# Kernel optimization log

Hardware: AMD Instinct MI355X
Metric: run time of the kernel (lower is better)

Reference implementation:

```python
import jax, jax.numpy as jnp
import numpy as np

N_NODES = 50000
N_EDGES = 800000
IN_CH = 128
HID = 128
NUM_GRAPHS = 512
BN_EPS = 1e-5


def setup_inputs() -> dict:
    key = jax.random.key(0)
    ks = jax.random.split(key, 16)
    x = jax.random.normal(ks[0], (N_NODES, IN_CH), dtype=jnp.float32)
    edge_index = jax.random.randint(ks[1], (2, N_EDGES), 0, N_NODES, dtype=jnp.int64)
    batch = jnp.sort(jax.random.randint(ks[2], (N_NODES,), 0, NUM_GRAPHS, dtype=jnp.int64))

    def glorot(k, shape):
        fan_in = shape[1]
        return jax.random.normal(k, shape, dtype=jnp.float32) / jnp.sqrt(jnp.float32(fan_in))

    # SAGEConv1: lin_l (aggr path, with bias), lin_r (root path, no bias)
    W1l = glorot(ks[3], (HID, IN_CH)); b1 = jnp.zeros((HID,), jnp.float32)
    W1r = glorot(ks[4], (HID, IN_CH))
    # SAGEConv2
    W2l = glorot(ks[5], (HID, HID)); b2 = jnp.zeros((HID,), jnp.float32)
    W2r = glorot(ks[6], (HID, HID))
    # MLP tail
    lin1_w = glorot(ks[7], (HID, HID)); lin1_b = jnp.zeros((HID,), jnp.float32)
    lin2_w = glorot(ks[8], (2, HID)); lin2_b = jnp.zeros((2,), jnp.float32)
    # BatchNorm1d (eval mode, running stats)
    gamma = jnp.ones((HID,), jnp.float32)
    beta = jnp.zeros((HID,), jnp.float32)
    running_mean = jax.random.normal(ks[9], (HID,), dtype=jnp.float32) * 0.1
    running_var = jax.random.uniform(ks[10], (HID,), dtype=jnp.float32, minval=0.5, maxval=1.5)
    return {
        "x": x, "edge_index": edge_index, "batch": batch,
        "W1l": W1l, "b1": b1, "W1r": W1r,
        "W2l": W2l, "b2": b2, "W2r": W2r,
        "lin1_w": lin1_w, "lin1_b": lin1_b,
        "lin2_w": lin2_w, "lin2_b": lin2_b,
        "gamma": gamma, "beta": beta,
        "running_mean": running_mean, "running_var": running_var,
    }


def _sage_conv(x, src, dst, Wl, bl, Wr):
    # mean-aggregate neighbor features (message flows src -> dst)
    n = x.shape[0]
    agg = jax.ops.segment_sum(x[src], dst, num_segments=n)  # [N, d]
    cnt = jax.ops.segment_sum(jnp.ones((src.shape[0], 1), x.dtype), dst, num_segments=n)
    mean = agg / jnp.maximum(cnt, 1.0)
    return mean @ Wl.T + bl + x @ Wr.T


def reference(x, edge_index, batch, W1l, b1, W1r, W2l, b2, W2r,
              lin1_w, lin1_b, lin2_w, lin2_b, gamma, beta,
              running_mean, running_var):
    src, dst = edge_index[0], edge_index[1]
    h = _sage_conv(x, src, dst, W1l, b1, W1r)      # [N, HID]
    h = _sage_conv(h, src, dst, W2l, b2, W2r)      # [N, HID]
    h = jax.ops.segment_sum(h, batch, num_segments=NUM_GRAPHS)  # global_add_pool -> [G, HID]
    h = h @ lin1_w.T + lin1_b
    # BatchNorm1d in eval mode (running stats)
    h = (h - running_mean) * jax.lax.rsqrt(running_var + BN_EPS) * gamma + beta
    h = jax.nn.relu(h)
    h = h @ lin2_w.T + lin2_b                      # [G, 2]
    # Dropout is identity in eval mode
    return h
```

## Files before the change

### kernel.cpp

```cpp
#include <hip/hip_runtime.h>
#include <hip/hip_bf16.h>

#define NN 50000
#define NE 800000
#define HID 128
#define NG 512
#define BN_EPS 1e-5f

typedef __attribute__((ext_vector_type(8))) short bf16x8;
typedef __attribute__((ext_vector_type(4))) float f32x4;

__device__ __forceinline__ ushort f2bf(float f) {
    uint u = __float_as_uint(f);
    uint r = (u + 0x7fffu + ((u >> 16) & 1u)) >> 16;
    return (ushort)r;
}
__device__ __forceinline__ float bf_lo(uint v) { return __uint_as_float(v << 16); }
__device__ __forceinline__ float bf_hi(uint v) { return __uint_as_float(v & 0xffff0000u); }

#define HIST_BLOCKS 782
#define CONV_BLOCKS 6250
#define WPREP_BLOCKS 32
#define POOLZ_BLOCKS 64
#define PH_GRID (HIST_BLOCKS + CONV_BLOCKS + WPREP_BLOCKS + POOLZ_BLOCKS)

__global__ __launch_bounds__(256) void prep_hist_kernel(const int* __restrict__ ei,
                                                        int* __restrict__ deg,
                                                        int* __restrict__ rank,
                                                        const float* __restrict__ x,
                                                        ushort* __restrict__ xb,
                                                        const float* __restrict__ W0,
                                                        const float* __restrict__ W1,
                                                        const float* __restrict__ W2,
                                                        const float* __restrict__ W3,
                                                        ushort* __restrict__ Wp,
                                                        float* __restrict__ pooled) {
    uint b = blockIdx.x;
    if (b < HIST_BLOCKS) {
        int e4 = b * 256 + threadIdx.x;
        if (e4 < NE / 4) {
            int4 dst = ((const int4*)(ei + NE))[e4];
            int4 rk;
            rk.x = atomicAdd(&deg[dst.x], 1);
            rk.y = atomicAdd(&deg[dst.y], 1);
            rk.z = atomicAdd(&deg[dst.z], 1);
            rk.w = atomicAdd(&deg[dst.w], 1);
            ((int4*)rank)[e4] = rk;
        }
    } else if (b < HIST_BLOCKS + CONV_BLOCKS) {
        int i = (b - HIST_BLOCKS) * 256 + threadIdx.x;
        float4 v = ((const float4*)x)[i];
        ushort4 o;
        o.x = f2bf(v.x);
        o.y = f2bf(v.y);
        o.z = f2bf(v.z);
        o.w = f2bf(v.w);
        ((ushort4*)xb)[i] = o;
    } else if (b < HIST_BLOCKS + CONV_BLOCKS + WPREP_BLOCKS) {
        int wu = (b - HIST_BLOCKS - CONV_BLOCKS) * 4 + (threadIdx.x >> 6);
        if (wu >= 128) return;
        int lane = threadIdx.x & 63;
        int m = wu >> 5;
        int g = wu & 31;
        int tile = g >> 2;
        int chunk = g & 3;
        const float* W = (m == 0) ? W0 : (m == 1) ? W1 : (m == 2) ? W2 : W3;
        int col = tile * 16 + (lane & 15);
        int k0 = chunk * 32 + (lane >> 4) * 8;
        ushort* dst = Wp + ((size_t)wu * 64 + lane) * 8;
#pragma unroll
        for (int j = 0; j < 8; ++j) dst[j] = f2bf(W[col * HID + k0 + j]);
    } else {
        int i = (b - HIST_BLOCKS - CONV_BLOCKS - WPREP_BLOCKS) * 256 + threadIdx.x;
        ((float4*)pooled)[i] = make_float4(0.f, 0.f, 0.f, 0.f);
    }
}

__global__ __launch_bounds__(256) void scan1_kernel(const int* __restrict__ deg,
                                                    int* __restrict__ row_start,
                                                    int* __restrict__ bsums, int n) {
    __shared__ int wsum[4];
    int i = blockIdx.x * 256 + threadIdx.x;
    int lane = threadIdx.x & 63;
    int wid = threadIdx.x >> 6;
    int v = (i < n) ? deg[i] : 0;
    int sc = v;
#pragma unroll
    for (int off = 1; off < 64; off <<= 1) {
        int t = __shfl_up(sc, off);
        if (lane >= off) sc += t;
    }
    if (lane == 63) wsum[wid] = sc;
    __syncthreads();
    int wpre = 0;
#pragma unroll
    for (int k = 0; k < 4; ++k) wpre += (k < wid) ? wsum[k] : 0;
    if (i < n) row_start[i] = wpre + sc - v;
    if (threadIdx.x == 255) bsums[blockIdx.x] = wpre + sc;
}

__global__ __launch_bounds__(256) void scan23_kernel(int* __restrict__ row_start,
                                                     const int* __restrict__ bsums, int n) {
    __shared__ int sred[4];
    int v = (threadIdx.x < blockIdx.x) ? bsums[threadIdx.x] : 0;
#pragma unroll
    for (int off = 32; off > 0; off >>= 1) v += __shfl_xor(v, off);
    if ((threadIdx.x & 63) == 0) sred[threadIdx.x >> 6] = v;
    __syncthreads();
    int total = sred[0] + sred[1] + sred[2] + sred[3];
    int i = blockIdx.x * 256 + threadIdx.x;
    if (i < n) row_start[i] += total;
}

__global__ __launch_bounds__(256) void fill_kernel(const int* __restrict__ ei,
                                                   const int* __restrict__ row_start,
                                                   const int* __restrict__ rank,
                                                   ushort* __restrict__ srclist) {
    int e4 = blockIdx.x * 256 + threadIdx.x;
    if (e4 >= NE / 4) return;
    int4 src = ((const int4*)ei)[e4];
    int4 dst = ((const int4*)(ei + NE))[e4];
    int4 rk = ((const int4*)rank)[e4];
    int p0 = row_start[dst.x] + rk.x;
    int p1 = row_start[dst.y] + rk.y;
    int p2 = row_start[dst.z] + rk.z;
    int p3 = row_start[dst.w] + rk.w;
    srclist[p0] = (ushort)src.x;
    srclist[p1] = (ushort)src.y;
    srclist[p2] = (ushort)src.z;
    srclist[p3] = (ushort)src.w;
}

__global__ __launch_bounds__(256) void aggregate_kernel(const ushort* __restrict__ feat,
                                                        const int* __restrict__ row_start,
                                                        const int* __restrict__ deg,
                                                        const ushort* __restrict__ srclist,
                                                        ushort* __restrict__ mean, int n) {
    int node = blockIdx.x * 4 + (threadIdx.x >> 6);
    if (node >= n) return;
    int lane = threadIdx.x & 63;
    int cl = lane & 15;
    int sub = lane >> 4;
    const uint4* fb = (const uint4*)feat;
    int s0 = row_start[node];
    int d = deg[node];

    float a[8];
#pragma unroll
    for (int i = 0; i < 8; ++i) a[i] = 0.f;

    int j = 0;
    for (; j + 16 <= d; j += 16) {
        int i0 = srclist[s0 + j + sub];
        int i1 = srclist[s0 + j + 4 + sub];
        int i2 = srclist[s0 + j + 8 + sub];
        int i3 = srclist[s0 + j + 12 + sub];
        uint4 v0 = fb[(size_t)i0 * 16 + cl];
        uint4 v1 = fb[(size_t)i1 * 16 + cl];
        uint4 v2 = fb[(size_t)i2 * 16 + cl];
        uint4 v3 = fb[(size_t)i3 * 16 + cl];
        a[0] += (bf_lo(v0.x) + bf_lo(v1.x)) + (bf_lo(v2.x) + bf_lo(v3.x));
        a[1] += (bf_hi(v0.x) + bf_hi(v1.x)) + (bf_hi(v2.x) + bf_hi(v3.x));
        a[2] += (bf_lo(v0.y) + bf_lo(v1.y)) + (bf_lo(v2.y) + bf_lo(v3.y));
        a[3] += (bf_hi(v0.y) + bf_hi(v1.y)) + (bf_hi(v2.y) + bf_hi(v3.y));
        a[4] += (bf_lo(v0.z) + bf_lo(v1.z)) + (bf_lo(v2.z) + bf_lo(v3.z));
        a[5] += (bf_hi(v0.z) + bf_hi(v1.z)) + (bf_hi(v2.z) + bf_hi(v3.z));
        a[6] += (bf_lo(v0.w) + bf_lo(v1.w)) + (bf_lo(v2.w) + bf_lo(v3.w));
        a[7] += (bf_hi(v0.w) + bf_hi(v1.w)) + (bf_hi(v2.w) + bf_hi(v3.w));
    }
    if (j < d) {
        int dm1 = d - 1;
        int k0 = j + sub;
        int k1 = j + 4 + sub;
        int k2 = j + 8 + sub;
        int k3 = j + 12 + sub;
        int i0 = srclist[s0 + min(k0, dm1)];
        int i1 = srclist[s0 + min(k1, dm1)];
        int i2 = srclist[s0 + min(k2, dm1)];
        int i3 = srclist[s0 + min(k3, dm1)];
        uint4 v0 = fb[(size_t)i0 * 16 + cl];
        uint4 v1 = fb[(size_t)i1 * 16 + cl];
        uint4 v2 = fb[(size_t)i2 * 16 + cl];
        uint4 v3 = fb[(size_t)i3 * 16 + cl];
        float m0 = (k0 < d) ? 1.f : 0.f;
        float m1 = (k1 < d) ? 1.f : 0.f;
        float m2 = (k2 < d) ? 1.f : 0.f;
        float m3 = (k3 < d) ? 1.f : 0.f;
        a[0] += m0 * bf_lo(v0.x) + m1 * bf_lo(v1.x) + m2 * bf_lo(v2.x) + m3 * bf_lo(v3.x);
        a[1] += m0 * bf_hi(v0.x) + m1 * bf_hi(v1.x) + m2 * bf_hi(v2.x) + m3 * bf_hi(v3.x);
        a[2] += m0 * bf_lo(v0.y) + m1 * bf_lo(v1.y) + m2 * bf_lo(v2.y) + m3 * bf_lo(v3.y);
        a[3] += m0 * bf_hi(v0.y) + m1 * bf_hi(v1.y) + m2 * bf_hi(v2.y) + m3 * bf_hi(v3.y);
        a[4] += m0 * bf_lo(v0.z) + m1 * bf_lo(v1.z) + m2 * bf_lo(v2.z) + m3 * bf_lo(v3.z);
        a[5] += m0 * bf_hi(v0.z) + m1 * bf_hi(v1.z) + m2 * bf_hi(v2.z) + m3 * bf_hi(v3.z);
        a[6] += m0 * bf_lo(v0.w) + m1 * bf_lo(v1.w) + m2 * bf_lo(v2.w) + m3 * bf_lo(v3.w);
        a[7] += m0 * bf_hi(v0.w) + m1 * bf_hi(v1.w) + m2 * bf_hi(v2.w) + m3 * bf_hi(v3.w);
    }

#pragma unroll
    for (int i = 0; i < 8; ++i) {
        float v = a[i];
        v += __shfl_xor(v, 16);
        v += __shfl_xor(v, 32);
        a[i] = v;
    }

    if (sub == 0) {
        float inv = 1.0f / fmaxf((float)d, 1.0f);
        uint4 o;
        o.x = (uint)f2bf(a[0] * inv) | ((uint)f2bf(a[1] * inv) << 16);
        o.y = (uint)f2bf(a[2] * inv) | ((uint)f2bf(a[3] * inv) << 16);
        o.z = (uint)f2bf(a[4] * inv) | ((uint)f2bf(a[5] * inv) << 16);
        o.w = (uint)f2bf(a[6] * inv) | ((uint)f2bf(a[7] * inv) << 16);
        ((uint4*)mean)[(size_t)node * 16 + cl] = o;
    }
}

template <bool POOL>
__global__ __launch_bounds__(256) void sage_gemm_mfma(const ushort* __restrict__ Amean,
                                                      const ushort* __restrict__ Aroot,
                                                      const ushort* __restrict__ WpL,
                                                      const float* __restrict__ bias,
                                                      const int* __restrict__ batch,
                                                      void* __restrict__ outv, int nwaves) {
    int w = blockIdx.x * 4 + (threadIdx.x >> 6);
    if (w >= nwaves) return;
    int lane = threadIdx.x & 63;
    int mrow = lane & 15;
    int quad = lane >> 4;
    int r0 = w * 16;

    f32x4 acc[8];
#pragma unroll
    for (int t = 0; t < 8; ++t) acc[t] = (f32x4){0.f, 0.f, 0.f, 0.f};

    const ushort* arow_m = Amean + ((size_t)(r0 + mrow)) * HID + quad * 8;
    const ushort* arow_r = Aroot + ((size_t)(r0 + mrow)) * HID + quad * 8;

#pragma unroll
    for (int half = 0; half < 2; ++half) {
        const ushort* arow = half ? arow_r : arow_m;
        const ushort* wb = WpL + (size_t)half * 16384 + (size_t)lane * 8;
#pragma unroll
        for (int c = 0; c < 4; ++c) {
            bf16x8 a = *(const bf16x8*)(arow + c * 32);
#pragma unroll
            for (int t = 0; t < 8; ++t) {
                bf16x8 b = *(const bf16x8*)(wb + (size_t)(t * 4 + c) * 512);
                acc[t] = __builtin_amdgcn_mfma_f32_16x16x32_bf16(a, b, acc[t], 0, 0, 0);
            }
        }
    }

    if (POOL) {
        float* pooled = (float*)outv;
        int rbase = r0 + quad * 4;
        int g0 = batch[rbase + 0];
        int g1 = batch[rbase + 1];
        int g2 = batch[rbase + 2];
        int g3 = batch[rbase + 3];
#pragma unroll
        for (int t = 0; t < 8; ++t) {
            int col = t * 16 + mrow;
            float bv = bias[col];
            float v0 = acc[t][0] + bv;
            float v1 = acc[t][1] + bv;
            float v2 = acc[t][2] + bv;
            float v3 = acc[t][3] + bv;
            int cg = g0;
            float s = v0;
            if (g1 == cg) s += v1; else { atomicAdd(&pooled[(size_t)cg * HID + col], s); cg = g1; s = v1; }
            if (g2 == cg) s += v2; else { atomicAdd(&pooled[(size_t)cg * HID + col], s); cg = g2; s = v2; }
            if (g3 == cg) s += v3; else { atomicAdd(&pooled[(size_t)cg * HID + col], s); cg = g3; s = v3; }
            atomicAdd(&pooled[(size_t)cg * HID + col], s);
        }
    } else {
        ushort* out = (ushort*)outv;
#pragma unroll
        for (int t = 0; t < 8; ++t) {
            int col = t * 16 + mrow;
            float bv = bias[col];
#pragma unroll
            for (int r = 0; r < 4; ++r) {
                int row = r0 + quad * 4 + r;
                out[(size_t)row * HID + col] = f2bf(acc[t][r] + bv);
            }
        }
    }
}

__global__ __launch_bounds__(128) void tail_kernel(const float* __restrict__ pooled,
                                                   const float* __restrict__ lin1_w,
                                                   const float* __restrict__ lin1_b,
                                                   const float* __restrict__ lin2_w,
                                                   const float* __restrict__ lin2_b,
                                                   const float* __restrict__ gamma,
                                                   const float* __restrict__ beta,
                                                   const float* __restrict__ rmean,
                                                   const float* __restrict__ rvar,
                                                   float* __restrict__ out) {
    __shared__ float Wt[64 * 128];
    __shared__ float p[128];
    __shared__ float tbuf[128];
    int g = blockIdx.x;
    int c = threadIdx.x;
    p[c] = pooled[g * HID + c];
    float acc = lin1_b[c];
    int kk = c & 63;
    int chalf = c >> 6;
    for (int k0 = 0; k0 < 128; k0 += 64) {
        __syncthreads();
        for (int i = 0; i < 64; ++i) {
            int crow = i * 2 + chalf;
            float v = lin1_w[crow * HID + k0 + kk];
            Wt[kk * 128 + (crow ^ (kk & 31))] = v;
        }
        __syncthreads();
#pragma unroll
        for (int k = 0; k < 64; ++k) {
            acc += p[k0 + k] * Wt[k * 128 + (c ^ (k & 31))];
        }
    }
    float v = (acc - rmean[c]) * rsqrtf(rvar[c] + BN_EPS) * gamma[c] + beta[c];
    v = fmaxf(v, 0.f);
    tbuf[c] = v;
    __syncthreads();
    int j = c >> 6;
    int lane = c & 63;
    float partial = tbuf[lane] * lin2_w[j * HID + lane] +
                    tbuf[lane + 64] * lin2_w[j * HID + lane + 64];
    for (int off = 32; off > 0; off >>= 1) partial += __shfl_down(partial, off);
    if (lane == 0) out[g * 2 + j] = partial + lin2_b[j];
}

extern "C" void kernel_launch(void* const* d_in, const int* in_sizes, int n_in,
                              void* d_out, int out_size, void* d_ws, size_t ws_size,
                              hipStream_t stream) {
    const float* x = (const float*)d_in[0];
    const int* ei = (const int*)d_in[1];
    const int* batch = (const int*)d_in[2];
    const float* W1l = (const float*)d_in[3];
    const float* b1 = (const float*)d_in[4];
    const float* W1r = (const float*)d_in[5];
    const float* W2l = (const float*)d_in[6];
    const float* b2 = (const float*)d_in[7];
    const float* W2r = (const float*)d_in[8];
    const float* lin1_w = (const float*)d_in[9];
    const float* lin1_b = (const float*)d_in[10];
    const float* lin2_w = (const float*)d_in[11];
    const float* lin2_b = (const float*)d_in[12];
    const float* gamma = (const float*)d_in[13];
    const float* beta = (const float*)d_in[14];
    const float* rmean = (const float*)d_in[15];
    const float* rvar = (const float*)d_in[16];
    float* out = (float*)d_out;

    const int N = NN, E = NE;
    const int NWAVES = N / 16;

    char* p = (char*)d_ws;
    auto carve = [&](size_t bytes) {
        void* r = (void*)p;
        p += (bytes + 255) & ~(size_t)255;
        return r;
    };
    int* deg = (int*)carve((size_t)N * 4);
    int* row_start = (int*)carve((size_t)N * 4);
    int* bsums = (int*)carve(1024 * 4);
    int* rank = (int*)carve((size_t)E * 4);
    ushort* srclist = (ushort*)carve((size_t)E * 2 + 64);
    ushort* xb = (ushort*)carve((size_t)N * HID * 2);
    ushort* meanb = (ushort*)carve((size_t)N * HID * 2);
    ushort* h1 = (ushort*)carve((size_t)N * HID * 2);
    float* pooled = (float*)carve((size_t)NG * HID * 4);
    ushort* Wp = (ushort*)carve(4 * 32 * 64 * 8 * 2);

    hipMemsetAsync(deg, 0, (size_t)N * 4, stream);

    prep_hist_kernel<<<PH_GRID, 256, 0, stream>>>(ei, deg, rank, x, xb,
                                                  W1l, W1r, W2l, W2r, Wp, pooled);

    const int scanBlocks = (N + 255) / 256;
    scan1_kernel<<<scanBlocks, 256, 0, stream>>>(deg, row_start, bsums, N);
    scan23_kernel<<<scanBlocks, 256, 0, stream>>>(row_start, bsums, N);
    fill_kernel<<<(E / 4 + 255) / 256, 256, 0, stream>>>(ei, row_start, rank, srclist);

    aggregate_kernel<<<(N + 3) / 4, 256, 0, stream>>>(xb, row_start, deg, srclist, meanb, N);
    sage_gemm_mfma<false><<<(NWAVES + 3) / 4, 256, 0, stream>>>(meanb, xb, Wp, b1, nullptr, h1,
                                                                NWAVES);
    aggregate_kernel<<<(N + 3) / 4, 256, 0, stream>>>(h1, row_start, deg, srclist, meanb, N);
    sage_gemm_mfma<true><<<(NWAVES + 3) / 4, 256, 0, stream>>>(meanb, h1, Wp + 32768, b2, batch,
                                                               pooled, NWAVES);
    tail_kernel<<<NG, 128, 0, stream>>>(pooled, lin1_w, lin1_b, lin2_w, lin2_b,
                                        gamma, beta, rmean, rvar, out);
}
```

Baseline: 259.2 us.

## Replace global atomic degree histogram with per-chunk shared-memory histograms

The edge-degree histogram now runs as 128 blocks, each counting a 12500-edge chunk over half the node range. Counts are packed as 16-bit pairs in LDS (50KB per block), so the global atomics and the memset of deg go away. A new chunkscan kernel does a column-wise prefix over the 64 chunks to produce per-chunk offsets and total degrees, and fill adds the chunk offset to the rank. This trades contended global atomics for an extra kernel and a 6.4MB offset table. The large static LDS array is also allocated by the conversion and weight-prep blocks, which may reduce their occupancy.

```diff
diff --git a/kernel.cpp b/kernel.cpp
--- a/kernel.cpp
+++ b/kernel.cpp
@@ -18,15 +18,19 @@
 __device__ __forceinline__ float bf_lo(uint v) { return __uint_as_float(v << 16); }
 __device__ __forceinline__ float bf_hi(uint v) { return __uint_as_float(v & 0xffff0000u); }
 
-#define HIST_BLOCKS 782
+#define NCH 64
+#define CHE 12500
+#define HRNG 25000
+#define HWORDS 12500
+#define HIST_BLOCKS 128
 #define CONV_BLOCKS 6250
 #define WPREP_BLOCKS 32
 #define POOLZ_BLOCKS 64
 #define PH_GRID (HIST_BLOCKS + CONV_BLOCKS + WPREP_BLOCKS + POOLZ_BLOCKS)
 
 __global__ __launch_bounds__(256) void prep_hist_kernel(const int* __restrict__ ei,
-                                                        int* __restrict__ deg,
-                                                        int* __restrict__ rank,
+                                                        ushort* __restrict__ rank,
+                                                        ushort* __restrict__ blockcnt,
                                                         const float* __restrict__ x,
                                                         ushort* __restrict__ xb,
                                                         const float* __restrict__ W0,
@@ -35,18 +39,27 @@
                                                         const float* __restrict__ W3,
                                                         ushort* __restrict__ Wp,
                                                         float* __restrict__ pooled) {
+    __shared__ uint hh[HWORDS];
     uint b = blockIdx.x;
     if (b < HIST_BLOCKS) {
-        int e4 = b * 256 + threadIdx.x;
-        if (e4 < NE / 4) {
-            int4 dst = ((const int4*)(ei + NE))[e4];
-            int4 rk;
-            rk.x = atomicAdd(&deg[dst.x], 1);
-            rk.y = atomicAdd(&deg[dst.y], 1);
-            rk.z = atomicAdd(&deg[dst.z], 1);
-            rk.w = atomicAdd(&deg[dst.w], 1);
-            ((int4*)rank)[e4] = rk;
-        }
+        int c = b >> 1;
+        int r = b & 1;
+        for (int i = threadIdx.x; i < HWORDS; i += 256) hh[i] = 0;
+        __syncthreads();
+        int base = c * CHE;
+        int lo = r * HRNG;
+        for (int k = threadIdx.x; k < CHE; k += 256) {
+            int d = ei[NE + base + k];
+            int local = d - lo;
+            if ((unsigned)local < (unsigned)HRNG) {
+                uint sh = (local & 1) << 4;
+                uint old = atomicAdd(&hh[local >> 1], 1u << sh);
+                rank[base + k] = (ushort)((old >> sh) & 0xffffu);
+            }
+        }
+        __syncthreads();
+        uint* dstw = (uint*)(blockcnt + (size_t)c * NN) + r * HWORDS;
+        for (int i = threadIdx.x; i < HWORDS; i += 256) dstw[i] = hh[i];
     } else if (b < HIST_BLOCKS + CONV_BLOCKS) {
         int i = (b - HIST_BLOCKS) * 256 + threadIdx.x;
         float4 v = ((const float4*)x)[i];
@@ -76,6 +89,22 @@
     }
 }
 
+__global__ __launch_bounds__(256) void chunkscan_kernel(ushort* __restrict__ blockcnt,
+                                                        int* __restrict__ deg) {
+    int t = blockIdx.x * 256 + threadIdx.x;
+    if (t >= NN / 2) return;
+    uint run_lo = 0, run_hi = 0;
+    uint* col = (uint*)blockcnt + t;
+#pragma unroll 4
+    for (int c = 0; c < NCH; ++c) {
+        uint w = col[(size_t)c * (NN / 2)];
+        col[(size_t)c * (NN / 2)] = run_lo | (run_hi << 16);
+        run_lo += w & 0xffffu;
+        run_hi += w >> 16;
+    }
+    ((int2*)deg)[t] = make_int2((int)run_lo, (int)run_hi);
+}
+
 __global__ __launch_bounds__(256) void scan1_kernel(const int* __restrict__ deg,
                                                     int* __restrict__ row_start,
                                                     int* __restrict__ bsums, int n) {
@@ -114,17 +143,20 @@
 
 __global__ __launch_bounds__(256) void fill_kernel(const int* __restrict__ ei,
                                                    const int* __restrict__ row_start,
-                                                   const int* __restrict__ rank,
+                                                   const ushort* __restrict__ rank,
+                                                   const ushort* __restrict__ blockcnt,
                                                    ushort* __restrict__ srclist) {
     int e4 = blockIdx.x * 256 + threadIdx.x;
     if (e4 >= NE / 4) return;
     int4 src = ((const int4*)ei)[e4];
     int4 dst = ((const int4*)(ei + NE))[e4];
-    int4 rk = ((const int4*)rank)[e4];
-    int p0 = row_start[dst.x] + rk.x;
-    int p1 = row_start[dst.y] + rk.y;
-    int p2 = row_start[dst.z] + rk.z;
-    int p3 = row_start[dst.w] + rk.w;
+    ushort4 rk = ((const ushort4*)rank)[e4];
+    int c = e4 / (CHE / 4);
+    const ushort* off = blockcnt + (size_t)c * NN;
+    int p0 = row_start[dst.x] + off[dst.x] + rk.x;
+    int p1 = row_start[dst.y] + off[dst.y] + rk.y;
+    int p2 = row_start[dst.z] + off[dst.z] + rk.z;
+    int p3 = row_start[dst.w] + off[dst.w] + rk.w;
     srclist[p0] = (ushort)src.x;
     srclist[p1] = (ushort)src.y;
     srclist[p2] = (ushort)src.z;
@@ -366,7 +398,8 @@
     int* deg = (int*)carve((size_t)N * 4);
     int* row_start = (int*)carve((size_t)N * 4);
     int* bsums = (int*)carve(1024 * 4);
-    int* rank = (int*)carve((size_t)E * 4);
+    ushort* rank = (ushort*)carve((size_t)E * 2);
+    ushort* blockcnt = (ushort*)carve((size_t)NCH * NN * 2);
     ushort* srclist = (ushort*)carve((size_t)E * 2 + 64);
     ushort* xb = (ushort*)carve((size_t)N * HID * 2);
     ushort* meanb = (ushort*)carve((size_t)N * HID * 2);
@@ -374,15 +407,15 @@
     float* pooled = (float*)carve((size_t)NG * HID * 4);
     ushort* Wp = (ushort*)carve(4 * 32 * 64 * 8 * 2);
 
-    hipMemsetAsync(deg, 0, (size_t)N * 4, stream);
-
-    prep_hist_kernel<<<PH_GRID, 256, 0, stream>>>(ei, deg, rank, x, xb,
+    prep_hist_kernel<<<PH_GRID, 256, 0, stream>>>(ei, rank, blockcnt, x, xb,
                                                   W1l, W1r, W2l, W2r, Wp, pooled);
+
+    chunkscan_kernel<<<(N / 2 + 255) / 256, 256, 0, stream>>>(blockcnt, deg);
 
     const int scanBlocks = (N + 255) / 256;
     scan1_kernel<<<scanBlocks, 256, 0, stream>>>(deg, row_start, bsums, N);
     scan23_kernel<<<scanBlocks, 256, 0, stream>>>(row_start, bsums, N);
-    fill_kernel<<<(E / 4 + 255) / 256, 256, 0, stream>>>(ei, row_start, rank, srclist);
+    fill_kernel<<<(E / 4 + 255) / 256, 256, 0, stream>>>(ei, row_start, rank, blockcnt, srclist);
 
     aggregate_kernel<<<(N + 3) / 4, 256, 0, stream>>>(xb, row_start, deg, srclist, meanb, N);
     sage_gemm_mfma<false><<<(NWAVES + 3) / 4, 256, 0, stream>>>(meanb, xb, Wp, b1, nullptr, h1,
```

Result: faster. 251.7 us (-2.9%).
